# Optimization experiments

Hardware: AMD Instinct MI355X
Metric: run time of the kernel (lower is better)

## Reference

```python
import jax, jax.numpy as jnp
import numpy as np

DIM = 512
NUM_HEADS = 8


def setup_inputs() -> dict:
    key = jax.random.key(0)
    ks = jax.random.split(key, 10)
    B, N, C = 2, 4096, DIM
    s = 0.02
    return {
        "x": jax.random.normal(ks[0], (B, N, C), dtype=jnp.float32),
        "Wq": jax.random.normal(ks[1], (C, C), dtype=jnp.float32) * s,
        "Wk": jax.random.normal(ks[2], (C, C), dtype=jnp.float32) * s,
        "Wv": jax.random.normal(ks[3], (C, C), dtype=jnp.float32) * s,
        "Wattn": jax.random.normal(ks[4], (C, C), dtype=jnp.float32) * s,
        "Wconv": jax.random.normal(ks[5], (C, C), dtype=jnp.float32) * s,
        "dw_kernel": jax.random.normal(ks[6], (C, 1, 3), dtype=jnp.float32) * s,  # depthwise (O, I/groups, K)
        "dw_bias": jax.random.normal(ks[7], (C,), dtype=jnp.float32) * s,
        "Wcout": jax.random.normal(ks[8], (C, C), dtype=jnp.float32) * s,
        "H": 8,
        "W": 512,
    }


def reference(x, Wq, Wk, Wv, Wattn, Wconv, dw_kernel, dw_bias, Wcout, H, W):
    B, N, C = x.shape
    nh = NUM_HEADS
    hd = C // nh
    scale = hd ** (-0.5)

    # QKV projections (torch Linear: x @ W.T), split heads -> [B, nh, N, hd]
    q = (x @ Wq.T).reshape(B, N, nh, hd).transpose(0, 2, 1, 3)
    k = (x @ Wk.T).reshape(B, N, nh, hd).transpose(0, 2, 1, 3)
    v = (x @ Wv.T).reshape(B, N, nh, hd).transpose(0, 2, 1, 3)

    # Materialized N x N attention (faithful to source)
    scores = jnp.einsum("bhqd,bhkd->bhqk", q, k) * scale
    weights = jax.nn.softmax(scores, axis=-1)
    attn = jnp.einsum("bhqk,bhkd->bhqd", weights, v)
    attn = attn.transpose(0, 2, 1, 3).reshape(B, N, C)
    attn_out = attn @ Wattn.T

    # Parallel depthwise-conv branch
    ci = (x @ Wconv.T).transpose(0, 2, 1)  # [B, C, N]
    co = jax.lax.conv_general_dilated(
        ci, dw_kernel,
        window_strides=(1,), padding=((1, 1),),
        feature_group_count=C,
        dimension_numbers=("NCH", "OIH", "NCH"),
    ) + dw_bias[None, :, None]
    conv_out = co.transpose(0, 2, 1) @ Wcout.T  # [B, N, C]

    out = attn_out + conv_out
    # NOTE: source shadows arg H with num_heads before the view
    return out.reshape(B, nh, W, C)
```

## Files before the change

### kernel.cpp

```cpp
#include <hip/hip_runtime.h>

typedef __attribute__((ext_vector_type(8))) short bf16x8;
typedef __attribute__((ext_vector_type(4))) float f32x4;

constexpr int kB = 2, kN = 4096, kC = 512, kNH = 8, kHD = 64;
constexpr int kBN = kB * kN;
constexpr int kWElems = 262144;
constexpr int kWAll = 6 * kWElems;
constexpr int kWExtra = 3584;
constexpr float kQScale = 0.1803368801f;

__device__ __forceinline__ short f2bf(float f) {
  union { float f; unsigned u; } v; v.f = f;
  unsigned r = v.u + 0x7fffu + ((v.u >> 16) & 1u);
  return (short)(r >> 16);
}
__device__ __forceinline__ float bf2f(short s) {
  union { unsigned u; float f; } v; v.u = ((unsigned)(unsigned short)s) << 16;
  return v.f;
}
__device__ __forceinline__ float exp2_(float x) {
#if __has_builtin(__builtin_amdgcn_exp2f)
  return __builtin_amdgcn_exp2f(x);
#else
  return exp2f(x);
#endif
}
__device__ __forceinline__ unsigned pk2bf(float a, float b) {
  union { float f; unsigned u; } ua, ub; ua.f = a; ub.f = b;
#if __has_builtin(__builtin_amdgcn_perm)
  return __builtin_amdgcn_perm(ub.u + 0x8000u, ua.u + 0x8000u, 0x07060302u);
#else
  return ((ua.u + 0x8000u) >> 16) | (((ub.u + 0x8000u) >> 16) << 16);
#endif
}

__device__ __forceinline__ bf16x8 ld8(const short* p) { return *(const bf16x8*)p; }
__device__ __forceinline__ bf16x8 ld8(const float* p) {
  float4 a = *(const float4*)p;
  float4 b = *(const float4*)(p + 4);
  bf16x8 r;
  r[0] = f2bf(a.x); r[1] = f2bf(a.y); r[2] = f2bf(a.z); r[3] = f2bf(a.w);
  r[4] = f2bf(b.x); r[5] = f2bf(b.y); r[6] = f2bf(b.z); r[7] = f2bf(b.w);
  return r;
}
__device__ __forceinline__ void stf(short* p, float v) { *p = f2bf(v); }
__device__ __forceinline__ void stf(float* p, float v) { *p = v; }

__device__ __forceinline__ void gload_lds16(const void* g, void* l) {
  __builtin_amdgcn_global_load_lds(
      (const __attribute__((address_space(1))) void*)g,
      (__attribute__((address_space(3))) void*)l, 16, 0, 0);
}

__global__ void detect_dtype(const unsigned* __restrict__ x, int* __restrict__ flag) {
  const int lane = threadIdx.x & 63;
  unsigned w = x[lane];
  int e = (int)((w >> 7) & 0xffu);
  bool bf = (e >= 100 && e <= 140);
  unsigned long long m = __ballot(bf);
  if (lane == 0) *flag = (__popcll(m) >= 32) ? 1 : 0;
}

constexpr int kW8 = kWAll / 8;
constexpr int kX8 = kBN * kC / 8;
__global__ __launch_bounds__(256) void convert_all(
    const void* Wq, const void* Wk, const void* Wv, const void* Wc,
    const void* Wa, const void* Wco, const void* dwk, const void* dwb,
    const void* x, const int* __restrict__ flag, short* __restrict__ dst,
    short* __restrict__ xb) {
  const int gtid = blockIdx.x * 256 + threadIdx.x;
  const bool bf = (*flag != 0);
  if (gtid < kW8) {
    const int e = gtid * 8;
    const int t = e >> 18, off = e & (kWElems - 1);
    const void* src = (t == 0) ? Wq : (t == 1) ? Wk : (t == 2) ? Wv
                    : (t == 3) ? Wc : (t == 4) ? Wa : Wco;
    bf16x8 v = bf ? ld8((const short*)src + off) : ld8((const float*)src + off);
    *(bf16x8*)(dst + e) = v;
  } else if (gtid < kW8 + kWExtra) {
    const int eoff = gtid - kW8;
    if (eoff < 1536) {
      dst[kWAll + eoff] = bf ? ((const short*)dwk)[eoff]
                             : f2bf(((const float*)dwk)[eoff]);
    } else if (eoff < 2048) {
      const int i = eoff - 1536;
      dst[kWAll + 1536 + i] = bf ? ((const short*)dwb)[i]
                                 : f2bf(((const float*)dwb)[i]);
    } else {
      const int t2 = eoff - 2048;
      const int tap = t2 >> 9, c = t2 & 511;
      dst[kWAll + 2048 + t2] = bf ? ((const short*)dwk)[c * 3 + tap]
                                  : f2bf(((const float*)dwk)[c * 3 + tap]);
    }
  } else if (gtid < kW8 + kWExtra + kX8) {
    const int e = (gtid - kW8 - kWExtra) * 8;
    bf16x8 v = bf ? ld8((const short*)x + e) : ld8((const float*)x + e);
    *(bf16x8*)(xb + e) = v;
  }
}

__global__ __launch_bounds__(256, 3) void proj_gemm(
    const short* __restrict__ xb, const short* __restrict__ wb,
    short* __restrict__ q, short* __restrict__ k, short* __restrict__ vT,
    short* __restrict__ ci) {
  __shared__ __align__(16) short As[128 * 64];
  __shared__ __align__(16) short Bs[128 * 64];
  const int t = threadIdx.x;
  const int wave = t >> 6, lane = t & 63;
  const int row = lane & 15, quad = lane >> 4;
  const int bn = blockIdx.x & 15;
  const int bm = blockIdx.x >> 4;
  const int m0 = bm * 128, n0 = bn * 128;
  const int wm = wave & 1, wn = wave >> 1;
  const int lrow = lane >> 3, lch = lane & 7;

  f32x4 acc[4][4];
#pragma unroll
  for (int mi = 0; mi < 4; ++mi)
#pragma unroll
    for (int ni = 0; ni < 4; ++ni)
#pragma unroll
      for (int r = 0; r < 4; ++r) acc[mi][ni][r] = 0.0f;

  for (int k0 = 0; k0 < kC; k0 += 64) {
#pragma unroll
    for (int p = 0; p < 4; ++p) {
      const int m = wave * 32 + p * 8 + lrow;
      const int kch = lch ^ (m & 7);
      gload_lds16(xb + (size_t)(m0 + m) * kC + k0 + kch * 8,
                  &As[(wave * 32 + p * 8) * 64]);
      gload_lds16(wb + (size_t)(n0 + m) * kC + k0 + kch * 8,
                  &Bs[(wave * 32 + p * 8) * 64]);
    }
    __syncthreads();

#pragma unroll
    for (int kk2 = 0; kk2 < 2; ++kk2) {
      bf16x8 af[4], bfr[4];
#pragma unroll
      for (int mi = 0; mi < 4; ++mi) {
        const int m = wm * 64 + mi * 16 + row;
        const int ch = (kk2 * 4 + quad) ^ (m & 7);
        af[mi] = *(const bf16x8*)(&As[m * 64 + ch * 8]);
      }
#pragma unroll
      for (int ni = 0; ni < 4; ++ni) {
        const int n = wn * 64 + ni * 16 + row;
        const int ch = (kk2 * 4 + quad) ^ (n & 7);
        bfr[ni] = *(const bf16x8*)(&Bs[n * 64 + ch * 8]);
      }
#pragma unroll
      for (int mi = 0; mi < 4; ++mi)
#pragma unroll
        for (int ni = 0; ni < 4; ++ni)
          acc[mi][ni] = __builtin_amdgcn_mfma_f32_16x16x32_bf16(
              af[mi], bfr[ni], acc[mi][ni], 0, 0, 0);
    }
    __syncthreads();
  }

  const int gc0 = n0 + wn * 64;
  const int mat = gc0 >> 9;
  const float scale = (mat == 0) ? kQScale : 1.0f;
#pragma unroll
  for (int mi = 0; mi < 4; ++mi) {
#pragma unroll
    for (int ni = 0; ni < 4; ++ni) {
#pragma unroll
      for (int r = 0; r < 4; ++r) {
        const int gm = m0 + wm * 64 + mi * 16 + quad * 4 + r;
        const int c_ = ((gc0 + ni * 16) & 511) + row;
        const int b_ = gm >> 12;
        const int n_ = gm & (kN - 1);
        const short bv = f2bf(acc[mi][ni][r] * scale);
        if (mat == 3) {
          ci[(b_ * kN + n_) * kC + c_] = bv;
        } else {
          const int h = c_ >> 6, d = c_ & 63;
          const int bh = b_ * kNH + h;
          if (mat == 0)      q[(bh * kN + n_) * kHD + d] = bv;
          else if (mat == 1) k[(bh * kN + n_) * kHD + d] = bv;
          else               vT[(bh * kHD + d) * kN + n_] = bv;
        }
      }
    }
  }
}

__global__ __launch_bounds__(256) void dwconv(
    const short* __restrict__ ci, const short* __restrict__ wb,
    short* __restrict__ cb) {
  const int e0 = (blockIdx.x * 256 + threadIdx.x) * 8;
  const int c0 = e0 & (kC - 1);
  const int bn = e0 >> 9;
  const int n_ = bn & (kN - 1);
  bf16x8 xc = ld8(ci + e0);
  bf16x8 xm, xp;
  if (n_ > 0) xm = ld8(ci + e0 - kC);
  else
#pragma unroll
    for (int i = 0; i < 8; ++i) xm[i] = 0;
  if (n_ < kN - 1) xp = ld8(ci + e0 + kC);
  else
#pragma unroll
    for (int i = 0; i < 8; ++i) xp[i] = 0;
  bf16x8 w0 = ld8(wb + kWAll + 2048 + c0);
  bf16x8 w1 = ld8(wb + kWAll + 2048 + 512 + c0);
  bf16x8 w2 = ld8(wb + kWAll + 2048 + 1024 + c0);
  bf16x8 bi = ld8(wb + kWAll + 1536 + c0);
  bf16x8 o;
#pragma unroll
  for (int i = 0; i < 8; ++i) {
    float a = bf2f(bi[i]) + bf2f(xm[i]) * bf2f(w0[i]) +
              bf2f(xc[i]) * bf2f(w1[i]) + bf2f(xp[i]) * bf2f(w2[i]);
    o[i] = f2bf(a);
  }
  *(bf16x8*)(cb + e0) = o;
}

__global__ __launch_bounds__(256, 2) void attn_flash(
    const short* __restrict__ q, const short* __restrict__ k,
    const short* __restrict__ vT, short* __restrict__ attn) {
  __shared__ __align__(16) short Kb[2][2][64 * 64];
  __shared__ __align__(16) short VbS[2][2][64 * 72];
  const int t = threadIdx.x;
  const int wave = t >> 6;
  const int lane = t & 63;
  const int row = lane & 15;
  const int quad = lane >> 4;

  const int slot = blockIdx.x & 7;
  const int inner = blockIdx.x >> 3;
  const int bh = slot * 2 + (inner & 1);
  const int q0 = (inner >> 1) * 128 + wave * 32;

  const short* qbase = q + (size_t)(bh * kN + q0) * kHD;
  const short* kbase = k + (size_t)bh * kN * kHD;
  const short* vbase = vT + (size_t)bh * kHD * kN;

  bf16x8 qb[2][2];
#pragma unroll
  for (int g = 0; g < 2; ++g) {
    qb[g][0] = *(const bf16x8*)(qbase + (g * 16 + row) * kHD + quad * 8);
    qb[g][1] = *(const bf16x8*)(qbase + (g * 16 + row) * kHD + 32 + quad * 8);
  }

  f32x4 o[2][4];
#pragma unroll
  for (int g = 0; g < 2; ++g)
#pragma unroll
    for (int j = 0; j < 4; ++j)
#pragma unroll
      for (int r = 0; r < 4; ++r) o[g][j][r] = 0.0f;
  float l_[2] = {0.0f, 0.0f};

  const int ksrow = lane >> 3;
  const int kschunk = (lane & 7) ^ ksrow;

  const int i0 = t, i1 = t + 256;
  const int sr0 = i0 >> 3, sc0 = i0 & 7;
  const int sr1 = i1 >> 3, sc1 = i1 & 7;
  const int vb0 = (sc0 >> 2) * 32 + (sc0 & 1) * 16 + (sc0 & 2) * 2;
  const int vb1 = (sc1 >> 2) * 32 + (sc1 & 1) * 16 + (sc1 & 2) * 2;

  auto stage_v = [&](int ph, int tl, bf16x8 v0, bf16x8 v1) {
    *(short4*)(&VbS[ph][tl][sr0 * 72 + vb0]) =
        make_short4(v0[0], v0[1], v0[2], v0[3]);
    *(short4*)(&VbS[ph][tl][sr0 * 72 + vb0 + 8]) =
        make_short4(v0[4], v0[5], v0[6], v0[7]);
    *(short4*)(&VbS[ph][tl][sr1 * 72 + vb1]) =
        make_short4(v1[0], v1[1], v1[2], v1[3]);
    *(short4*)(&VbS[ph][tl][sr1 * 72 + vb1 + 8]) =
        make_short4(v1[4], v1[5], v1[6], v1[7]);
  };
  auto stage_k = [&](int ph, int kt2) {
#pragma unroll
    for (int tl = 0; tl < 2; ++tl)
#pragma unroll
      for (int j = 0; j < 2; ++j)
        gload_lds16(
            kbase + (size_t)((kt2 + tl) * 64 + j * 32 + wave * 8 + ksrow) * 64 +
                kschunk * 8,
            &Kb[ph][tl][j * 2048 + wave * 512]);
  };

  const int c0s = ((quad) ^ (row & 7)) * 8;
  const int c1s = ((quad + 4) ^ (row & 7)) * 8;

  auto tile_step = [&](const short* kt_base, const short* vt_base) {
    f32x4 s[2][4];
#pragma unroll
    for (int g = 0; g < 2; ++g)
#pragma unroll
      for (int jk = 0; jk < 4; ++jk)
#pragma unroll
        for (int r = 0; r < 4; ++r) s[g][jk][r] = 0.0f;
    __builtin_amdgcn_s_setprio(1);
#pragma unroll
    for (int jk = 0; jk < 4; ++jk) {
      const short* kr = kt_base + (jk * 16 + row) * 64;
      bf16x8 a0 = *(const bf16x8*)(kr + c0s);
      bf16x8 a1 = *(const bf16x8*)(kr + c1s);
#pragma unroll
      for (int g = 0; g < 2; ++g) {
        s[g][jk] = __builtin_amdgcn_mfma_f32_16x16x32_bf16(a0, qb[g][0], s[g][jk], 0, 0, 0);
        s[g][jk] = __builtin_amdgcn_mfma_f32_16x16x32_bf16(a1, qb[g][1], s[g][jk], 0, 0, 0);
      }
    }
    __builtin_amdgcn_s_setprio(0);

    bf16x8 pb[2][2];
#pragma unroll
    for (int g = 0; g < 2; ++g) {
      float tj[4];
#pragma unroll
      for (int jk = 0; jk < 4; ++jk) {
#pragma unroll
        for (int r = 0; r < 4; ++r) s[g][jk][r] = exp2_(s[g][jk][r]);
        tj[jk] = (s[g][jk][0] + s[g][jk][1]) + (s[g][jk][2] + s[g][jk][3]);
      }
      l_[g] += (tj[0] + tj[1]) + (tj[2] + tj[3]);
#pragma unroll
      for (int c = 0; c < 2; ++c) {
        union { unsigned u[4]; bf16x8 v; } pu;
        pu.u[0] = pk2bf(s[g][2 * c][0], s[g][2 * c][1]);
        pu.u[1] = pk2bf(s[g][2 * c][2], s[g][2 * c][3]);
        pu.u[2] = pk2bf(s[g][2 * c + 1][0], s[g][2 * c + 1][1]);
        pu.u[3] = pk2bf(s[g][2 * c + 1][2], s[g][2 * c + 1][3]);
        pb[g][c] = pu.v;
      }
    }

    __builtin_amdgcn_s_setprio(1);
#pragma unroll
    for (int jd = 0; jd < 4; ++jd) {
      const short* vb = vt_base + (jd * 16 + row) * 72 + quad * 8;
#pragma unroll
      for (int c = 0; c < 2; ++c) {
        bf16x8 av = *(const bf16x8*)(vb + c * 32);
#pragma unroll
        for (int g = 0; g < 2; ++g)
          o[g][jd] = __builtin_amdgcn_mfma_f32_16x16x32_bf16(
              av, pb[g][c], o[g][jd], 0, 0, 0);
      }
    }
    __builtin_amdgcn_s_setprio(0);
  };

  {
    stage_k(0, 0);
    bf16x8 a = *(const bf16x8*)(vbase + sr0 * kN + sc0 * 8);
    bf16x8 b = *(const bf16x8*)(vbase + sr1 * kN + sc1 * 8);
    stage_v(0, 0, a, b);
    a = *(const bf16x8*)(vbase + sr0 * kN + 64 + sc0 * 8);
    b = *(const bf16x8*)(vbase + sr1 * kN + 64 + sc1 * 8);
    stage_v(0, 1, a, b);
  }
  __syncthreads();

  for (int p = 0; p < 32; ++p) {
    const int cur = p & 1;
    const bool more = (p < 31);
    bf16x8 vn00, vn01, vn10, vn11;
    if (more) {
      const int kk = (2 * p + 2) * 64;
      stage_k(1 - cur, 2 * p + 2);
      vn00 = *(const bf16x8*)(vbase + sr0 * kN + kk + sc0 * 8);
      vn01 = *(const bf16x8*)(vbase + sr1 * kN + kk + sc1 * 8);
      vn10 = *(const bf16x8*)(vbase + sr0 * kN + kk + 64 + sc0 * 8);
      vn11 = *(const bf16x8*)(vbase + sr1 * kN + kk + 64 + sc1 * 8);
    }

    tile_step(&Kb[cur][0][0], &VbS[cur][0][0]);

    if (more) {
      stage_v(1 - cur, 0, vn00, vn01);
      stage_v(1 - cur, 1, vn10, vn11);
    }

    tile_step(&Kb[cur][1][0], &VbS[cur][1][0]);
    __syncthreads();
  }

  const int b_ = bh >> 3, h = bh & 7;
#pragma unroll
  for (int g = 0; g < 2; ++g) {
    float lt = l_[g];
    lt += __shfl_xor(lt, 16);
    lt += __shfl_xor(lt, 32);
    const float linv = 1.0f / lt;
    const int n_ = q0 + g * 16 + row;
    short* ob = attn + (size_t)(b_ * kN + n_) * kC + h * kHD + quad * 4;
#pragma unroll
    for (int jd = 0; jd < 4; ++jd) {
      short4 st = make_short4(f2bf(o[g][jd][0] * linv), f2bf(o[g][jd][1] * linv),
                              f2bf(o[g][jd][2] * linv), f2bf(o[g][jd][3] * linv));
      *(short4*)(ob + jd * 16) = st;
    }
  }
}

template <typename TO>
__device__ __forceinline__ void out_body(
    const short* __restrict__ attn, const short* __restrict__ cb,
    const short* __restrict__ wb, TO* __restrict__ out) {
  __shared__ __align__(16) short As[128 * 64];
  __shared__ __align__(16) short Bs[64 * 64];
  const int t = threadIdx.x;
  const int wave = t >> 6, lane = t & 63;
  const int row = lane & 15, quad = lane >> 4;
  const int bn = blockIdx.x & 7;
  const int bm = blockIdx.x >> 3;
  const int m0 = bm * 128, n0 = bn * 64;
  const int wm = wave & 1, wn = wave >> 1;
  const int lrow = lane >> 3, lch = lane & 7;

  f32x4 acc[4][2];
#pragma unroll
  for (int mi = 0; mi < 4; ++mi)
#pragma unroll
    for (int ni = 0; ni < 2; ++ni)
#pragma unroll
      for (int r = 0; r < 4; ++r) acc[mi][ni][r] = 0.0f;

  const short* Wa = wb + 4 * kWElems;
  const short* Wo = wb + 5 * kWElems;

  for (int k0 = 0; k0 < 1024; k0 += 64) {
    const short* Asrc = (k0 < 512) ? attn : cb;
    const short* Bsrc = (k0 < 512) ? Wa : Wo;
    const int ka = k0 & 511;
#pragma unroll
    for (int p = 0; p < 4; ++p) {
      const int m = wave * 32 + p * 8 + lrow;
      const int kch = lch ^ (m & 7);
      gload_lds16(Asrc + (size_t)(m0 + m) * kC + ka + kch * 8,
                  &As[(wave * 32 + p * 8) * 64]);
    }
#pragma unroll
    for (int p = 0; p < 2; ++p) {
      const int n = wave * 16 + p * 8 + lrow;
      const int kch = lch ^ (n & 7);
      gload_lds16(Bsrc + (size_t)(n0 + n) * kC + ka + kch * 8,
                  &Bs[(wave * 16 + p * 8) * 64]);
    }
    __syncthreads();

#pragma unroll
    for (int kk2 = 0; kk2 < 2; ++kk2) {
      bf16x8 af[4], bfr[2];
#pragma unroll
      for (int mi = 0; mi < 4; ++mi) {
        const int m = wm * 64 + mi * 16 + row;
        const int ch = (kk2 * 4 + quad) ^ (m & 7);
        af[mi] = *(const bf16x8*)(&As[m * 64 + ch * 8]);
      }
#pragma unroll
      for (int ni = 0; ni < 2; ++ni) {
        const int n = wn * 32 + ni * 16 + row;
        const int ch = (kk2 * 4 + quad) ^ (n & 7);
        bfr[ni] = *(const bf16x8*)(&Bs[n * 64 + ch * 8]);
      }
#pragma unroll
      for (int mi = 0; mi < 4; ++mi)
#pragma unroll
        for (int ni = 0; ni < 2; ++ni)
          acc[mi][ni] = __builtin_amdgcn_mfma_f32_16x16x32_bf16(
              af[mi], bfr[ni], acc[mi][ni], 0, 0, 0);
    }
    __syncthreads();
  }

#pragma unroll
  for (int mi = 0; mi < 4; ++mi)
#pragma unroll
    for (int ni = 0; ni < 2; ++ni)
#pragma unroll
      for (int r = 0; r < 4; ++r) {
        const int gm = m0 + wm * 64 + mi * 16 + quad * 4 + r;
        const int gc = n0 + wn * 32 + ni * 16 + row;
        stf(out + (size_t)gm * kC + gc, acc[mi][ni][r]);
      }
}

__global__ __launch_bounds__(256, 4) void out_gemm(
    const short* __restrict__ attn, const short* __restrict__ cb,
    const short* __restrict__ wb, const int* __restrict__ flag, void* out) {
  if (*flag)
    out_body<short>(attn, cb, wb, (short*)out);
  else
    out_body<float>(attn, cb, wb, (float*)out);
}

extern "C" void kernel_launch(void* const* d_in, const int* in_sizes, int n_in,
                              void* d_out, int out_size, void* d_ws, size_t ws_size,
                              hipStream_t stream) {
  const void* x   = d_in[0];
  const void* Wq  = d_in[1];
  const void* Wk  = d_in[2];
  const void* Wv  = d_in[3];
  const void* Wa  = d_in[4];
  const void* Wc  = d_in[5];
  const void* dwk = d_in[6];
  const void* dwb = d_in[7];
  const void* Wco = d_in[8];

  short* ws = (short*)d_ws;
  const size_t E = (size_t)kBN * kC;
  int*   flag = (int*)ws;
  short* wb   = ws + 256;
  short* q    = wb + kWAll + kWExtra;
  short* k    = q + E;
  short* vT   = k + E;
  short* ci   = vT + E;
  short* cb   = ci + E;
  short* attn = ci;
  short* xb   = cb;

  detect_dtype<<<1, 64, 0, stream>>>((const unsigned*)x, flag);
  const int cvt_threads = kW8 + kWExtra + kX8;
  convert_all<<<(cvt_threads + 255) / 256, 256, 0, stream>>>(
      Wq, Wk, Wv, Wc, Wa, Wco, dwk, dwb, x, flag, wb, xb);
  proj_gemm<<<1024, 256, 0, stream>>>(xb, wb, q, k, vT, ci);
  dwconv<<<(kBN * kC) / (256 * 8), 256, 0, stream>>>(ci, wb, cb);
  attn_flash<<<512, 256, 0, stream>>>(q, k, vT, attn);
  out_gemm<<<512, 256, 0, stream>>>(attn, cb, wb, flag, d_out);
}
```

Measured before the change: 259.2 us.

## Split keys across two wave groups in flash attention and merge via LDS

The attention block grows from 4 to 8 waves. Each group of 4 waves processes half of the key/value sequence for the same 128 queries, with each half staged into its own LDS slot per iteration. After the loop, the second group writes its partial O and row sums to reused LDS, and the first group adds them in before normalising and storing. This doubles the waves per block for better latency hiding at the same LDS footprint, in exchange for an extra reduction pass and higher register pressure under the new launch bounds.

```diff
diff --git a/kernel.cpp b/kernel.cpp
--- a/kernel.cpp
+++ b/kernel.cpp
@@ -219,7 +219,7 @@
   *(bf16x8*)(cb + e0) = o;
 }
 
-__global__ __launch_bounds__(256, 2) void attn_flash(
+__global__ __launch_bounds__(512, 4) void attn_flash(
     const short* __restrict__ q, const short* __restrict__ k,
     const short* __restrict__ vT, short* __restrict__ attn) {
   __shared__ __align__(16) short Kb[2][2][64 * 64];
@@ -229,11 +229,13 @@
   const int lane = t & 63;
   const int row = lane & 15;
   const int quad = lane >> 4;
+  const int qg = wave & 3;
+  const int ks = wave >> 2;
 
   const int slot = blockIdx.x & 7;
   const int inner = blockIdx.x >> 3;
   const int bh = slot * 2 + (inner & 1);
-  const int q0 = (inner >> 1) * 128 + wave * 32;
+  const int q0 = (inner >> 1) * 128 + qg * 32;
 
   const short* qbase = q + (size_t)(bh * kN + q0) * kHD;
   const short* kbase = k + (size_t)bh * kN * kHD;
@@ -257,32 +259,32 @@
 
   const int ksrow = lane >> 3;
   const int kschunk = (lane & 7) ^ ksrow;
-
-  const int i0 = t, i1 = t + 256;
+  auto stage_k = [&](int buf, int kt) {
+#pragma unroll
+    for (int s2 = 0; s2 < 2; ++s2)
+      gload_lds16(
+          kbase + (size_t)(s2 * 2048 + kt * 64 + wave * 8 + ksrow) * 64 +
+              kschunk * 8,
+          &Kb[buf][s2][wave * 512]);
+  };
+
+  const int sv = t >> 8;
+  const int ii = t & 255;
+  const int i0 = ii, i1 = ii + 256;
   const int sr0 = i0 >> 3, sc0 = i0 & 7;
   const int sr1 = i1 >> 3, sc1 = i1 & 7;
   const int vb0 = (sc0 >> 2) * 32 + (sc0 & 1) * 16 + (sc0 & 2) * 2;
   const int vb1 = (sc1 >> 2) * 32 + (sc1 & 1) * 16 + (sc1 & 2) * 2;
 
-  auto stage_v = [&](int ph, int tl, bf16x8 v0, bf16x8 v1) {
-    *(short4*)(&VbS[ph][tl][sr0 * 72 + vb0]) =
+  auto stage_v = [&](int buf, bf16x8 v0, bf16x8 v1) {
+    *(short4*)(&VbS[buf][sv][sr0 * 72 + vb0]) =
         make_short4(v0[0], v0[1], v0[2], v0[3]);
-    *(short4*)(&VbS[ph][tl][sr0 * 72 + vb0 + 8]) =
+    *(short4*)(&VbS[buf][sv][sr0 * 72 + vb0 + 8]) =
         make_short4(v0[4], v0[5], v0[6], v0[7]);
-    *(short4*)(&VbS[ph][tl][sr1 * 72 + vb1]) =
+    *(short4*)(&VbS[buf][sv][sr1 * 72 + vb1]) =
         make_short4(v1[0], v1[1], v1[2], v1[3]);
-    *(short4*)(&VbS[ph][tl][sr1 * 72 + vb1 + 8]) =
+    *(short4*)(&VbS[buf][sv][sr1 * 72 + vb1 + 8]) =
         make_short4(v1[4], v1[5], v1[6], v1[7]);
-  };
-  auto stage_k = [&](int ph, int kt2) {
-#pragma unroll
-    for (int tl = 0; tl < 2; ++tl)
-#pragma unroll
-      for (int j = 0; j < 2; ++j)
-        gload_lds16(
-            kbase + (size_t)((kt2 + tl) * 64 + j * 32 + wave * 8 + ksrow) * 64 +
-                kschunk * 8,
-            &Kb[ph][tl][j * 2048 + wave * 512]);
   };
 
   const int c0s = ((quad) ^ (row & 7)) * 8;
@@ -350,53 +352,68 @@
 
   {
     stage_k(0, 0);
-    bf16x8 a = *(const bf16x8*)(vbase + sr0 * kN + sc0 * 8);
-    bf16x8 b = *(const bf16x8*)(vbase + sr1 * kN + sc1 * 8);
-    stage_v(0, 0, a, b);
-    a = *(const bf16x8*)(vbase + sr0 * kN + 64 + sc0 * 8);
-    b = *(const bf16x8*)(vbase + sr1 * kN + 64 + sc1 * 8);
-    stage_v(0, 1, a, b);
+    bf16x8 a = *(const bf16x8*)(vbase + (size_t)sr0 * kN + sv * 2048 + sc0 * 8);
+    bf16x8 b = *(const bf16x8*)(vbase + (size_t)sr1 * kN + sv * 2048 + sc1 * 8);
+    stage_v(0, a, b);
   }
   __syncthreads();
 
-  for (int p = 0; p < 32; ++p) {
-    const int cur = p & 1;
-    const bool more = (p < 31);
-    bf16x8 vn00, vn01, vn10, vn11;
+  for (int kt = 0; kt < 32; ++kt) {
+    const int cur = kt & 1;
+    const bool more = (kt < 31);
+    bf16x8 vn0, vn1;
     if (more) {
-      const int kk = (2 * p + 2) * 64;
-      stage_k(1 - cur, 2 * p + 2);
-      vn00 = *(const bf16x8*)(vbase + sr0 * kN + kk + sc0 * 8);
-      vn01 = *(const bf16x8*)(vbase + sr1 * kN + kk + sc1 * 8);
-      vn10 = *(const bf16x8*)(vbase + sr0 * kN + kk + 64 + sc0 * 8);
-      vn11 = *(const bf16x8*)(vbase + sr1 * kN + kk + 64 + sc1 * 8);
-    }
-
-    tile_step(&Kb[cur][0][0], &VbS[cur][0][0]);
-
-    if (more) {
-      stage_v(1 - cur, 0, vn00, vn01);
-      stage_v(1 - cur, 1, vn10, vn11);
-    }
-
-    tile_step(&Kb[cur][1][0], &VbS[cur][1][0]);
+      stage_k(1 - cur, kt + 1);
+      const int off = sv * 2048 + (kt + 1) * 64;
+      vn0 = *(const bf16x8*)(vbase + (size_t)sr0 * kN + off + sc0 * 8);
+      vn1 = *(const bf16x8*)(vbase + (size_t)sr1 * kN + off + sc1 * 8);
+    }
+
+    tile_step(&Kb[cur][ks][0], &VbS[cur][ks][0]);
+
+    if (more) stage_v(1 - cur, vn0, vn1);
     __syncthreads();
   }
 
-  const int b_ = bh >> 3, h = bh & 7;
-#pragma unroll
-  for (int g = 0; g < 2; ++g) {
-    float lt = l_[g];
-    lt += __shfl_xor(lt, 16);
-    lt += __shfl_xor(lt, 32);
-    const float linv = 1.0f / lt;
-    const int n_ = q0 + g * 16 + row;
-    short* ob = attn + (size_t)(b_ * kN + n_) * kC + h * kHD + quad * 4;
-#pragma unroll
-    for (int jd = 0; jd < 4; ++jd) {
-      short4 st = make_short4(f2bf(o[g][jd][0] * linv), f2bf(o[g][jd][1] * linv),
-                              f2bf(o[g][jd][2] * linv), f2bf(o[g][jd][3] * linv));
-      *(short4*)(ob + jd * 16) = st;
+  float* Of = (float*)&Kb[0][0][0];
+  float* Lf = (float*)&VbS[0][0][0];
+  if (ks == 1) {
+#pragma unroll
+    for (int g = 0; g < 2; ++g) {
+#pragma unroll
+      for (int jd = 0; jd < 4; ++jd)
+#pragma unroll
+        for (int r = 0; r < 4; ++r)
+          Of[(g * 16 + jd * 4 + r) * 256 + qg * 64 + lane] = o[g][jd][r];
+      Lf[g * 256 + qg * 64 + lane] = l_[g];
+    }
+  }
+  __syncthreads();
+  if (ks == 0) {
+#pragma unroll
+    for (int g = 0; g < 2; ++g) {
+#pragma unroll
+      for (int jd = 0; jd < 4; ++jd)
+#pragma unroll
+        for (int r = 0; r < 4; ++r)
+          o[g][jd][r] += Of[(g * 16 + jd * 4 + r) * 256 + qg * 64 + lane];
+      l_[g] += Lf[g * 256 + qg * 64 + lane];
+    }
+    const int b_ = bh >> 3, h = bh & 7;
+#pragma unroll
+    for (int g = 0; g < 2; ++g) {
+      float lt = l_[g];
+      lt += __shfl_xor(lt, 16);
+      lt += __shfl_xor(lt, 32);
+      const float linv = 1.0f / lt;
+      const int n_ = q0 + g * 16 + row;
+      short* ob = attn + (size_t)(b_ * kN + n_) * kC + h * kHD + quad * 4;
+#pragma unroll
+      for (int jd = 0; jd < 4; ++jd) {
+        short4 st = make_short4(f2bf(o[g][jd][0] * linv), f2bf(o[g][jd][1] * linv),
+                                f2bf(o[g][jd][2] * linv), f2bf(o[g][jd][3] * linv));
+        *(short4*)(ob + jd * 16) = st;
+      }
     }
   }
 }
@@ -524,6 +541,6 @@
       Wq, Wk, Wv, Wc, Wa, Wco, dwk, dwb, x, flag, wb, xb);
   proj_gemm<<<1024, 256, 0, stream>>>(xb, wb, q, k, vT, ci);
   dwconv<<<(kBN * kC) / (256 * 8), 256, 0, stream>>>(ci, wb, cb);
-  attn_flash<<<512, 256, 0, stream>>>(q, k, vT, attn);
+  attn_flash<<<512, 512, 0, stream>>>(q, k, vT, attn);
   out_gemm<<<512, 256, 0, stream>>>(attn, cb, wb, flag, d_out);
 }
```

After: 245.8 us. 1.05x faster.
